# Kernel optimization log

Hardware: AMD Instinct MI355X
Metric: run time of the kernel (lower is better)

Reference implementation:

```python
import jax, jax.numpy as jnp
import numpy as np

HEADS = 8
DIM_HEAD = 64
KNN = 32
SCALE = DIM_HEAD ** -0.5


def setup_inputs() -> dict:
    key = jax.random.key(0)
    k1, k2, k3 = jax.random.split(key, 3)
    B, N, C = 2, 2048, 256
    inner = HEADS * DIM_HEAD  # 512
    x = jax.random.normal(k1, (B, N, C), dtype=jnp.float32)
    Wqkv = jax.random.normal(k2, (C, 3 * inner), dtype=jnp.float32) * (C ** -0.5)
    Wout = jax.random.normal(k3, (inner, C), dtype=jnp.float32) * (inner ** -0.5)
    bout = jnp.zeros((C,), dtype=jnp.float32)
    return {"x": x, "Wqkv": Wqkv, "Wout": Wout, "bout": bout}


def _knn_adjacency(x, k):
    # x: [B, N, C] -> boolean adjacency [B, N, N], k nearest neighbors by
    # euclidean distance, self-loops excluded (loop=False).
    B, N, _ = x.shape
    x2 = jnp.sum(x * x, axis=-1)  # [B, N]
    # squared distances [B, N, N]
    d2 = x2[:, :, None] + x2[:, None, :] - 2.0 * jnp.einsum('bnc,bmc->bnm', x, x)
    big = jnp.finfo(d2.dtype).max
    d2 = d2 + big * jnp.eye(N, dtype=d2.dtype)  # exclude self
    _, idx = jax.lax.top_k(-d2, k)  # [B, N, k] nearest neighbor indices

    rows = jnp.arange(N)[:, None]  # [N, 1]

    def scatter_one(idx_b):
        return jnp.zeros((N, N), dtype=bool).at[rows, idx_b].set(True)

    return jax.vmap(scatter_one)(idx)  # [B, N, N]


def reference(x, Wqkv, Wout, bout):
    B, N, C = x.shape
    adj = _knn_adjacency(x, KNN)  # [B, N, N] bool, shared across heads

    qkv = x @ Wqkv  # [B, N, 3*inner]
    q, k, v = jnp.split(qkv, 3, axis=-1)
    split_heads = lambda t: t.reshape(B, N, HEADS, DIM_HEAD).transpose(0, 2, 1, 3)
    q, k, v = split_heads(q), split_heads(k), split_heads(v)  # [B, H, N, d]

    dots = jnp.einsum('bhnd,bhmd->bhnm', q, k) * SCALE  # [B, H, N, N]
    dots = jnp.where(adj[:, None, :, :], dots, -jnp.inf)
    attn = jax.nn.softmax(dots, axis=-1)
    out = jnp.einsum('bhnm,bhmd->bhnd', attn, v)  # [B, H, N, d]
    out = out.transpose(0, 2, 1, 3).reshape(B, N, HEADS * DIM_HEAD)
    return out @ Wout + bout
```

## Files before the change

kernel.cpp:

```cpp
#include <hip/hip_runtime.h>
#include <hip/hip_bf16.h>
#include <hip/hip_fp16.h>

#define BATCH 2
#define NPTS  2048
#define CDIM  256
#define NHEAD 8
#define DHEAD 64
#define INNER 512
#define TRIPLE 1536
#define KNN   32
#define SCALE 0.125f

#define GRAM_ITEMS 272
#define QKV_ITEMS  384
#define TOTAL_ITEMS (GRAM_ITEMS + QKV_ITEMS)

typedef __attribute__((ext_vector_type(8))) short short8;
typedef __attribute__((ext_vector_type(4))) float floatx4;
typedef __attribute__((ext_vector_type(4))) unsigned short ushort4v;
typedef unsigned short ushort;

#define TW  32
#define TSZ (128*TW)

__device__ __forceinline__ unsigned bfsplit(float x) {
    unsigned u = __float_as_uint(x);
    unsigned r = u + 0x7fffu + ((u >> 16) & 1u);
    unsigned hs = r >> 16;
    float hf = __uint_as_float(hs << 16);
    float lo = x - hf;
    unsigned u2 = __float_as_uint(lo);
    unsigned r2 = u2 + 0x7fffu + ((u2 >> 16) & 1u);
    return (hs & 0xffffu) | (r2 & 0xffff0000u);
}

__device__ __forceinline__ void bfsplit3(float x, ushort* hh, ushort* ll, ushort* qq) {
    unsigned u = __float_as_uint(x);
    unsigned r = u + 0x7fffu + ((u >> 16) & 1u);
    unsigned hs = r >> 16;
    float hf = __uint_as_float(hs << 16);
    float d1 = x - hf;
    unsigned u2 = __float_as_uint(d1);
    unsigned r2 = u2 + 0x7fffu + ((u2 >> 16) & 1u);
    unsigned ls = r2 >> 16;
    float lf = __uint_as_float(ls << 16);
    float d2 = d1 - lf;
    unsigned u3 = __float_as_uint(d2);
    unsigned r3 = u3 + 0x7fffu + ((u3 >> 16) & 1u);
    *hh = (ushort)hs;
    *ll = (ushort)ls;
    *qq = (ushort)(r3 >> 16);
}

__device__ __forceinline__ ushort f2h(float f) {
    __half h = __float2half(f);
    return *reinterpret_cast<ushort*>(&h);
}
__device__ __forceinline__ float h2f(ushort u) {
    __half h;
    *reinterpret_cast<ushort*>(&h) = u;
    return __half2float(h);
}

__global__ __launch_bounds__(256) void input_prep_kernel(const float* __restrict__ x,
                                                         float* __restrict__ x2,
                                                         ushort* __restrict__ xhi,
                                                         ushort* __restrict__ xlo,
                                                         ushort* __restrict__ xqd) {
    int wave = threadIdx.x >> 6, lane = threadIdx.x & 63;
    int row = blockIdx.x * 4 + wave;
    const float* xr = x + (size_t)row * CDIM;
    float4 v = *(const float4*)(xr + lane * 4);
    float s = v.x*v.x + v.y*v.y + v.z*v.z + v.w*v.w;
    #pragma unroll
    for (int o = 32; o; o >>= 1) s += __shfl_down(s, o);
    if (lane == 0) x2[row] = s;

    ushort h[4], l[4], q[4];
    bfsplit3(v.x, &h[0], &l[0], &q[0]);
    bfsplit3(v.y, &h[1], &l[1], &q[1]);
    bfsplit3(v.z, &h[2], &l[2], &q[2]);
    bfsplit3(v.w, &h[3], &l[3], &q[3]);
    size_t off = (size_t)row * CDIM + lane * 4;
    *(ushort4v*)(xhi + off) = *(ushort4v*)h;
    *(ushort4v*)(xlo + off) = *(ushort4v*)l;
    *(ushort4v*)(xqd + off) = *(ushort4v*)q;
}

__global__ __launch_bounds__(256) void wtrans2_kernel(const float* __restrict__ Wqkv,
                                                      const float* __restrict__ Wout,
                                                      ushort* __restrict__ wqhiT,
                                                      ushort* __restrict__ wqloT,
                                                      ushort* __restrict__ wohiT,
                                                      ushort* __restrict__ woloT) {
    __shared__ float tile[64][65];
    const float* W; ushort* hiT; ushort* loT; int K, N, bx, by;
    int bid = blockIdx.x;
    if (bid < 96) { W = Wqkv; hiT = wqhiT; loT = wqloT; K = CDIM;  N = TRIPLE; bx = bid % 24; by = bid / 24; }
    else { int t = bid - 96; W = Wout; hiT = wohiT; loT = woloT; K = INNER; N = CDIM;  bx = t % 4;  by = t / 4; }
    int k0 = by * 64, n0 = bx * 64;
    #pragma unroll
    for (int i = 0; i < 4; ++i) {
        int f = threadIdx.x + i * 256;
        int r = f >> 4, c4 = (f & 15) * 4;
        float4 v = *(const float4*)(W + (size_t)(k0 + r) * N + n0 + c4);
        tile[r][c4+0] = v.x; tile[r][c4+1] = v.y;
        tile[r][c4+2] = v.z; tile[r][c4+3] = v.w;
    }
    __syncthreads();
    #pragma unroll
    for (int i = 0; i < 4; ++i) {
        int f = threadIdx.x + i * 256;
        int rn = f >> 4, ck = (f & 15) * 4;
        unsigned p0 = bfsplit(tile[ck+0][rn]);
        unsigned p1 = bfsplit(tile[ck+1][rn]);
        unsigned p2 = bfsplit(tile[ck+2][rn]);
        unsigned p3 = bfsplit(tile[ck+3][rn]);
        ushort4v h, l;
        h.x = (ushort)p0; l.x = (ushort)(p0 >> 16);
        h.y = (ushort)p1; l.y = (ushort)(p1 >> 16);
        h.z = (ushort)p2; l.z = (ushort)(p2 >> 16);
        h.w = (ushort)p3; l.w = (ushort)(p3 >> 16);
        *(ushort4v*)(hiT + (size_t)(n0 + rn) * K + k0 + ck) = h;
        *(ushort4v*)(loT + (size_t)(n0 + rn) * K + k0 + ck) = l;
    }
}


__device__ __forceinline__ void gemm_split_body(const ushort* __restrict__ Ahi,
                                                const ushort* __restrict__ Alo,
                                                const ushort* __restrict__ BhiT,
                                                const ushort* __restrict__ BloT,
                                                const float* __restrict__ bias,
                                                float* __restrict__ C,
                                                int N, int K, int bi, int bj,
                                                ushort* lds,
                                                ushort* __restrict__ kv16) {
    int lane = threadIdx.x & 63, wave = threadIdx.x >> 6;
    int wr = wave >> 1, wc = wave & 1;
    int fr = lane & 15, kg = lane >> 4;
    int swz8 = (kg ^ ((fr >> 1) & 3)) * 8;

    int srow = threadIdx.x >> 1;
    int hc = (threadIdx.x & 1) * 2;
    int sw = (srow >> 1) & 3;
    int d0 = srow * TW + ((hc + 0) ^ sw) * 8;
    int d1 = srow * TW + ((hc + 1) ^ sw) * 8;

    const ushort* g0 = Ahi  + (size_t)(bi + srow) * K + hc * 8;
    const ushort* g1 = Alo  + (size_t)(bi + srow) * K + hc * 8;
    const ushort* g2 = BhiT + (size_t)(bj + srow) * K + hc * 8;
    const ushort* g3 = BloT + (size_t)(bj + srow) * K + hc * 8;

    floatx4 acc[4][4] = {};

    for (int k0 = 0; k0 < K; k0 += 32) {
        uint4 va0 = *(const uint4*)(g0 + k0);
        uint4 va1 = *(const uint4*)(g0 + k0 + 8);
        uint4 vb0 = *(const uint4*)(g1 + k0);
        uint4 vb1 = *(const uint4*)(g1 + k0 + 8);
        uint4 vc0 = *(const uint4*)(g2 + k0);
        uint4 vc1 = *(const uint4*)(g2 + k0 + 8);
        uint4 vd0 = *(const uint4*)(g3 + k0);
        uint4 vd1 = *(const uint4*)(g3 + k0 + 8);
        *(uint4*)&lds[0*TSZ + d0] = va0;  *(uint4*)&lds[0*TSZ + d1] = va1;
        *(uint4*)&lds[1*TSZ + d0] = vb0;  *(uint4*)&lds[1*TSZ + d1] = vb1;
        *(uint4*)&lds[2*TSZ + d0] = vc0;  *(uint4*)&lds[2*TSZ + d1] = vc1;
        *(uint4*)&lds[3*TSZ + d0] = vd0;  *(uint4*)&lds[3*TSZ + d1] = vd1;
        __syncthreads();

        short8 a_h[4], a_l[4], b_h[4], b_l[4];
        #pragma unroll
        for (int m = 0; m < 4; ++m) {
            int off = (wr*64 + m*16 + fr) * TW + swz8;
            a_h[m] = *(const short8*)&lds[0*TSZ + off];
            a_l[m] = *(const short8*)&lds[1*TSZ + off];
        }
        #pragma unroll
        for (int n = 0; n < 4; ++n) {
            int off = (wc*64 + n*16 + fr) * TW + swz8;
            b_h[n] = *(const short8*)&lds[2*TSZ + off];
            b_l[n] = *(const short8*)&lds[3*TSZ + off];
        }
        #pragma unroll
        for (int m = 0; m < 4; ++m)
            #pragma unroll
            for (int n = 0; n < 4; ++n) {
                acc[m][n] = __builtin_amdgcn_mfma_f32_16x16x32_bf16(a_h[m], b_h[n], acc[m][n], 0, 0, 0);
                acc[m][n] = __builtin_amdgcn_mfma_f32_16x16x32_bf16(a_h[m], b_l[n], acc[m][n], 0, 0, 0);
                acc[m][n] = __builtin_amdgcn_mfma_f32_16x16x32_bf16(a_l[m], b_h[n], acc[m][n], 0, 0, 0);
            }
        __syncthreads();
    }

    if (kv16) {
        bool is_q = (bj < INNER);
        #pragma unroll
        for (int m = 0; m < 4; ++m)
            #pragma unroll
            for (int n = 0; n < 4; ++n) {
                int col = bj + wc*64 + n*16 + fr;
                #pragma unroll
                for (int r = 0; r < 4; ++r) {
                    int row = bi + wr*64 + m*16 + kg*4 + r;
                    float val = acc[m][n][r];
                    if (is_q) C[(size_t)row * INNER + col] = val;
                    else      kv16[(size_t)row * 1024 + (col - INNER)] = f2h(val);
                }
            }
    } else {
        #pragma unroll
        for (int m = 0; m < 4; ++m)
            #pragma unroll
            for (int n = 0; n < 4; ++n) {
                int col = bj + wc*64 + n*16 + fr;
                float bv = bias ? bias[col] : 0.0f;
                #pragma unroll
                for (int r = 0; r < 4; ++r) {
                    int row = bi + wr*64 + m*16 + kg*4 + r;
                    C[(size_t)row * N + col] = acc[m][n][r] + bv;
                }
            }
    }
}

__device__ __forceinline__ void gram_body(const ushort* __restrict__ Ah,
                                          const ushort* __restrict__ Al,
                                          const ushort* __restrict__ Aq,
                                          const float* __restrict__ x2b,
                                          float* __restrict__ Sb,
                                          int bi, int bj, ushort* lds) {
    int lane = threadIdx.x & 63, wave = threadIdx.x >> 6;
    int wr = wave >> 1, wc = wave & 1;
    int fr = lane & 15, kg = lane >> 4;
    int swz8 = (kg ^ ((fr >> 1) & 3)) * 8;

    int srow = threadIdx.x >> 1;
    int hc = (threadIdx.x & 1) * 2;
    int sw = (srow >> 1) & 3;
    int d0 = srow * TW + ((hc + 0) ^ sw) * 8;
    int d1 = srow * TW + ((hc + 1) ^ sw) * 8;

    const ushort* g0 = Ah + (size_t)(bi + srow) * CDIM + hc * 8;
    const ushort* g1 = Al + (size_t)(bi + srow) * CDIM + hc * 8;
    const ushort* g2 = Aq + (size_t)(bi + srow) * CDIM + hc * 8;
    const ushort* g3 = Ah + (size_t)(bj + srow) * CDIM + hc * 8;
    const ushort* g4 = Al + (size_t)(bj + srow) * CDIM + hc * 8;
    const ushort* g5 = Aq + (size_t)(bj + srow) * CDIM + hc * 8;

    floatx4 acc[4][4] = {};

    for (int k0 = 0; k0 < CDIM; k0 += 32) {
        uint4 a0 = *(const uint4*)(g0 + k0); uint4 a1 = *(const uint4*)(g0 + k0 + 8);
        uint4 b0 = *(const uint4*)(g1 + k0); uint4 b1 = *(const uint4*)(g1 + k0 + 8);
        uint4 c0 = *(const uint4*)(g2 + k0); uint4 c1 = *(const uint4*)(g2 + k0 + 8);
        uint4 e0 = *(const uint4*)(g3 + k0); uint4 e1 = *(const uint4*)(g3 + k0 + 8);
        uint4 f0 = *(const uint4*)(g4 + k0); uint4 f1 = *(const uint4*)(g4 + k0 + 8);
        uint4 h0 = *(const uint4*)(g5 + k0); uint4 h1 = *(const uint4*)(g5 + k0 + 8);
        *(uint4*)&lds[0*TSZ + d0] = a0; *(uint4*)&lds[0*TSZ + d1] = a1;
        *(uint4*)&lds[1*TSZ + d0] = b0; *(uint4*)&lds[1*TSZ + d1] = b1;
        *(uint4*)&lds[2*TSZ + d0] = c0; *(uint4*)&lds[2*TSZ + d1] = c1;
        *(uint4*)&lds[3*TSZ + d0] = e0; *(uint4*)&lds[3*TSZ + d1] = e1;
        *(uint4*)&lds[4*TSZ + d0] = f0; *(uint4*)&lds[4*TSZ + d1] = f1;
        *(uint4*)&lds[5*TSZ + d0] = h0; *(uint4*)&lds[5*TSZ + d1] = h1;
        __syncthreads();

        short8 a_h[4], a_l[4], a_q[4], b_h[4], b_l[4], b_q[4];
        #pragma unroll
        for (int m = 0; m < 4; ++m) {
            int off = (wr*64 + m*16 + fr) * TW + swz8;
            a_h[m] = *(const short8*)&lds[0*TSZ + off];
            a_l[m] = *(const short8*)&lds[1*TSZ + off];
            a_q[m] = *(const short8*)&lds[2*TSZ + off];
        }
        #pragma unroll
        for (int n = 0; n < 4; ++n) {
            int off = (wc*64 + n*16 + fr) * TW + swz8;
            b_h[n] = *(const short8*)&lds[3*TSZ + off];
            b_l[n] = *(const short8*)&lds[4*TSZ + off];
            b_q[n] = *(const short8*)&lds[5*TSZ + off];
        }
        #pragma unroll
        for (int m = 0; m < 4; ++m)
            #pragma unroll
            for (int n = 0; n < 4; ++n) {
                acc[m][n] = __builtin_amdgcn_mfma_f32_16x16x32_bf16(a_h[m], b_h[n], acc[m][n], 0, 0, 0);
                acc[m][n] = __builtin_amdgcn_mfma_f32_16x16x32_bf16(a_h[m], b_l[n], acc[m][n], 0, 0, 0);
                acc[m][n] = __builtin_amdgcn_mfma_f32_16x16x32_bf16(a_l[m], b_h[n], acc[m][n], 0, 0, 0);
                acc[m][n] = __builtin_amdgcn_mfma_f32_16x16x32_bf16(a_l[m], b_l[n], acc[m][n], 0, 0, 0);
                acc[m][n] = __builtin_amdgcn_mfma_f32_16x16x32_bf16(a_h[m], b_q[n], acc[m][n], 0, 0, 0);
                acc[m][n] = __builtin_amdgcn_mfma_f32_16x16x32_bf16(a_q[m], b_h[n], acc[m][n], 0, 0, 0);
            }
        __syncthreads();
    }

    #pragma unroll
    for (int m = 0; m < 4; ++m)
        #pragma unroll
        for (int n = 0; n < 4; ++n) {
            int col = bj + wc*64 + n*16 + fr;
            float xc = x2b[col];
            #pragma unroll
            for (int r = 0; r < 4; ++r) {
                int row = bi + wr*64 + m*16 + kg*4 + r;
                float val = xc - 2.0f * acc[m][n][r];
                if (row == col) val = __builtin_inff();
                Sb[(size_t)row * NPTS + col] = val;
            }
        }

    if (bi != bj) {
        float* T = (float*)lds;
        #pragma unroll
        for (int p = 0; p < 2; ++p) {
            __syncthreads();
            if (wc == p) {
                #pragma unroll
                for (int m = 0; m < 4; ++m) {
                    int row0 = wr*64 + m*16 + kg*4;
                    float x0 = x2b[bi + row0 + 0];
                    float x1 = x2b[bi + row0 + 1];
                    float x2v = x2b[bi + row0 + 2];
                    float x3 = x2b[bi + row0 + 3];
                    #pragma unroll
                    for (int n = 0; n < 4; ++n) {
                        int colp = n*16 + fr;
                        float4 v;
                        v.x = x0 - 2.0f * acc[m][n][0];
                        v.y = x1 - 2.0f * acc[m][n][1];
                        v.z = x2v - 2.0f * acc[m][n][2];
                        v.w = x3 - 2.0f * acc[m][n][3];
                        *(float4*)&T[colp * 132 + row0] = v;
                    }
                }
            }
            __syncthreads();
            #pragma unroll
            for (int i = 0; i < 8; ++i) {
                int f = threadIdx.x + i * 256;
                int cr = f >> 5, c4 = (f & 31) * 4;
                float4 v = *(const float4*)&T[cr * 132 + c4];
                *(float4*)(Sb + (size_t)(bj + p*64 + cr) * NPTS + bi + c4) = v;
            }
        }
    }
}

__global__ __launch_bounds__(256) void fused_mfma_kernel(const ushort* __restrict__ xh,
                                                         const ushort* __restrict__ xl,
                                                         const ushort* __restrict__ xq,
                                                         const float* __restrict__ x2,
                                                         float* __restrict__ S,
                                                         const ushort* __restrict__ wqhiT,
                                                         const ushort* __restrict__ wqloT,
                                                         float* __restrict__ q,
                                                         ushort* __restrict__ kv16) {
    __shared__ ushort lds[6*TSZ];
    int item = blockIdx.x;
    if (item < GRAM_ITEMS) {
        int b = item / 136, t = item % 136;
        int by = 0;
        while (t >= 16 - by) { t -= 16 - by; ++by; }
        int bx = by + t;
        size_t xoff = (size_t)b * NPTS * CDIM;
        gram_body(xh + xoff, xl + xoff, xq + xoff,
                  x2 + (size_t)b * NPTS, S + (size_t)b * NPTS * NPTS,
                  by * 128, bx * 128, lds);
    } else {
        int t = item - GRAM_ITEMS;
        int bx = t % 12, by = t / 12;
        gemm_split_body(xh, xl, wqhiT, wqloT, nullptr, q,
                        TRIPLE, CDIM, by * 128, bx * 128, lds, kv16);
    }
}

__global__ __launch_bounds__(256) void outproj_kernel(const ushort* __restrict__ Ahi,
                                                      const ushort* __restrict__ Alo,
                                                      const ushort* __restrict__ BhiT,
                                                      const ushort* __restrict__ BloT,
                                                      const float* __restrict__ bias,
                                                      float* __restrict__ C) {
    __shared__ ushort lds[4*TSZ];
    gemm_split_body(Ahi, Alo, BhiT, BloT, bias, C,
                    CDIM, INNER, blockIdx.y * 128, blockIdx.x * 128, lds, nullptr);
}

__device__ __forceinline__ unsigned block_excl_scan_256(unsigned c,
                                                        unsigned* wsum,
                                                        unsigned* total_out) {
    unsigned v = c;
    #pragma unroll
    for (int o = 1; o < 64; o <<= 1) {
        unsigned t = __shfl_up(v, o);
        if ((threadIdx.x & 63) >= o) v += t;
    }
    if ((threadIdx.x & 63) == 63) wsum[threadIdx.x >> 6] = v;
    __syncthreads();
    unsigned woff = 0;
    int mywave = threadIdx.x >> 6;
    #pragma unroll
    for (int w = 0; w < 4; ++w) {
        unsigned s = wsum[w];
        if (w < mywave) woff += s;
    }
    if (total_out) *total_out = wsum[0] + wsum[1] + wsum[2] + wsum[3];
    __syncthreads();
    return v + woff - c;
}

__global__ __launch_bounds__(256) void knn_attn_kernel(const float* __restrict__ S,
                                                       const float* __restrict__ q,
                                                       const ushort* __restrict__ kv16,
                                                       ushort* __restrict__ ahi,
                                                       ushort* __restrict__ alo) {
    int bid = blockIdx.x;
    int b = (bid & 7) >> 2;
    int n = ((bid >> 3) << 2) | (bid & 3);
    size_t rowoff = (size_t)b * NPTS + n;
    const float* row = S + rowoff * NPTS;

    __shared__ unsigned keys[NPTS];
    __shared__ unsigned hist[256];
    __shared__ unsigned wsum[4];
    __shared__ unsigned s_red[8];
    __shared__ unsigned sh_lo, sh_hi, sh_rank, sh_cnt, sh_break;
    __shared__ unsigned ckey[64];
    __shared__ int     cidx[64];
    __shared__ unsigned s_ccount;
    __shared__ int   nb[KNN];
    __shared__ float dots[NHEAD][KNN];
    __shared__ float p[NHEAD][KNN];

    int tid = threadIdx.x;

    unsigned mn = 0xffffffffu, mx = 0u;
    {
        int i0 = tid * 8;
        float4 f0 = *(const float4*)(row + i0);
        float4 f1 = *(const float4*)(row + i0 + 4);
        float fv[8] = { f0.x, f0.y, f0.z, f0.w, f1.x, f1.y, f1.z, f1.w };
        #pragma unroll
        for (int t = 0; t < 8; ++t) {
            int i = i0 + t;
            unsigned u;
            if (i == n) {
                u = 0xffffffffu;
            } else {
                unsigned v = __float_as_uint(fv[t]);
                u = (v & 0x80000000u) ? ~v : (v | 0x80000000u);
                mn = min(mn, u); mx = max(mx, u);
            }
            keys[i] = u;
        }
    }
    #pragma unroll
    for (int o = 32; o; o >>= 1) {
        mn = min(mn, (unsigned)__shfl_xor((int)mn, o));
        mx = max(mx, (unsigned)__shfl_xor((int)mx, o));
    }
    if ((tid & 63) == 0) { s_red[tid >> 6] = mn; s_red[4 + (tid >> 6)] = mx; }
    __syncthreads();
    if (tid == 0) {
        unsigned a = min(min(s_red[0], s_red[1]), min(s_red[2], s_red[3]));
        unsigned z = max(max(s_red[4], s_red[5]), max(s_red[6], s_red[7]));
        sh_lo = a; sh_hi = z; sh_rank = KNN; sh_break = 0; s_ccount = 0;
    }
    __syncthreads();

    for (int it = 0; it < 5; ++it) {
        unsigned lo = sh_lo, hi = sh_hi;
        unsigned range1 = hi - lo;
        int shift = 0;
        if (range1 > 255u) shift = 24 - __clz(range1);
        hist[tid] = 0;
        __syncthreads();
        for (int i = tid; i < NPTS; i += 256) {
            unsigned u = keys[i];
            if (u >= lo && u <= hi)
                atomicAdd(&hist[(u - lo) >> shift], 1u);
        }
        __syncthreads();
        unsigned c = hist[tid];
        unsigned rank = sh_rank;
        unsigned excl = block_excl_scan_256(c, wsum, nullptr);
        if (excl < rank && excl + c >= rank) {
            sh_rank = rank - excl;
            unsigned nlo = lo + ((unsigned)tid << shift);
            unsigned span = (shift == 0) ? 0u : (((1u << shift)) - 1u);
            unsigned nhi = nlo + span;
            if (nhi > hi || nhi < nlo) nhi = hi;
            sh_lo = nlo; sh_hi = nhi;
            sh_cnt = c;
            sh_break = (shift == 0 || c <= 64u) ? 1u : 0u;
        }
        __syncthreads();
        if (sh_break) break;
    }

    unsigned lo = sh_lo, hi = sh_hi, rank = sh_rank, cnt = sh_cnt;

    unsigned lt = 0;
    for (int i = tid; i < NPTS; i += 256) lt += (keys[i] < lo) ? 1u : 0u;
    unsigned pos = block_excl_scan_256(lt, wsum, nullptr);
    for (int i = tid; i < NPTS; i += 256) {
        unsigned u = keys[i];
        if (u < lo) nb[pos++] = i;
        else if (u >= lo && u <= hi && cnt <= 64u) {
            unsigned pp = atomicAdd(&s_ccount, 1u);
            ckey[pp] = u; cidx[pp] = i;
        }
    }
    __syncthreads();

    unsigned base = KNN - rank;
    if (cnt <= 64u) {
        if (tid < (int)cnt) {
            unsigned myk = ckey[tid]; int myi = cidx[tid];
            unsigned r = 0;
            for (unsigned s = 0; s < cnt; ++s) {
                unsigned sk = ckey[s]; int si = cidx[s];
                r += (sk < myk || (sk == myk && si < myi)) ? 1u : 0u;
            }
            if (r < rank) nb[base + r] = myi;
        }
    } else {
        if (tid == 0) {
            unsigned need = rank, pp = base;
            for (int i = 0; i < NPTS && need; ++i) {
                if (keys[i] >= lo && keys[i] <= hi) { nb[pp++] = i; --need; }
            }
        }
    }
    __syncthreads();

    const float* qrow = q + rowoff * INNER;
    const ushort* kvb = kv16 + (size_t)b * NPTS * 1024;

    {
        int j = tid >> 3;
        int l = tid & 7;
        const ushort* krow = kvb + (size_t)nb[j] * 1024 + l * 8;
        short8 kr[NHEAD];
        #pragma unroll
        for (int h = 0; h < NHEAD; ++h)
            kr[h] = *(const short8*)(krow + h * DHEAD);
        const float* qp = qrow + l * 8;
        #pragma unroll
        for (int h = 0; h < NHEAD; ++h) {
            float4 q0 = *(const float4*)(qp + h * DHEAD);
            float4 q1 = *(const float4*)(qp + h * DHEAD + 4);
            float d = h2f((ushort)kr[h][0]) * q0.x + h2f((ushort)kr[h][1]) * q0.y
                    + h2f((ushort)kr[h][2]) * q0.z + h2f((ushort)kr[h][3]) * q0.w
                    + h2f((ushort)kr[h][4]) * q1.x + h2f((ushort)kr[h][5]) * q1.y
                    + h2f((ushort)kr[h][6]) * q1.z + h2f((ushort)kr[h][7]) * q1.w;
            d += __shfl_xor(d, 1);
            d += __shfl_xor(d, 2);
            d += __shfl_xor(d, 4);
            if (l == 0) dots[h][j] = d * SCALE;
        }
    }
    __syncthreads();

    {
        int h = tid >> 5, jj = tid & 31;
        float dv = dots[h][jj];
        float mxv = dv;
        for (int o = 16; o; o >>= 1) mxv = fmaxf(mxv, __shfl_xor(mxv, o));
        float e = expf(dv - mxv);
        float s = e;
        for (int o = 16; o; o >>= 1) s += __shfl_xor(s, o);
        p[h][jj] = e / s;
    }
    __syncthreads();

    {
        int hd = tid >> 5;
        int jd = tid & 31;
        const ushort* vb = kvb + INNER + hd * DHEAD + jd * 2;
        float o0 = 0.f, o1 = 0.f;
        #pragma unroll
        for (int g = 0; g < 4; ++g) {
            unsigned vv[8]; float pw[8];
            #pragma unroll
            for (int t = 0; t < 8; ++t) {
                int jj = g * 8 + t;
                vv[t] = *(const unsigned*)(vb + (size_t)nb[jj] * 1024);
                pw[t] = p[hd][jj];
            }
            #pragma unroll
            for (int t = 0; t < 8; ++t) {
                o0 += pw[t] * h2f((ushort)(vv[t] & 0xffffu));
                o1 += pw[t] * h2f((ushort)(vv[t] >> 16));
            }
        }
        size_t baseo = rowoff * INNER + hd * DHEAD + jd * 2;
        unsigned q0 = bfsplit(o0);
        unsigned q1 = bfsplit(o1);
        *(unsigned*)(ahi + baseo) = (q0 & 0xffffu) | (q1 << 16);
        *(unsigned*)(alo + baseo) = (q0 >> 16) | (q1 & 0xffff0000u);
    }
}

extern "C" void kernel_launch(void* const* d_in, const int* in_sizes, int n_in,
                              void* d_out, int out_size, void* d_ws, size_t ws_size,
                              hipStream_t stream) {
    const float* x    = (const float*)d_in[0];
    const float* Wqkv = (const float*)d_in[1];
    const float* Wout = (const float*)d_in[2];
    const float* bout = (const float*)d_in[3];
    float* out = (float*)d_out;

    float* S     = (float*)d_ws;
    float* x2    = S + (size_t)BATCH * NPTS * NPTS;
    float* q     = x2 + (size_t)BATCH * NPTS;
    ushort* kv16 = (ushort*)(q + (size_t)BATCH * NPTS * INNER);
    ushort* xhi  = kv16 + (size_t)BATCH * NPTS * 1024;
    ushort* xlo   = xhi   + (size_t)BATCH * NPTS * CDIM;
    ushort* xqd   = xlo   + (size_t)BATCH * NPTS * CDIM;
    ushort* ahi   = xqd   + (size_t)BATCH * NPTS * CDIM;
    ushort* alo   = ahi   + (size_t)BATCH * NPTS * INNER;
    ushort* wqhiT = alo   + (size_t)BATCH * NPTS * INNER;
    ushort* wqloT = wqhiT + (size_t)TRIPLE * CDIM;
    ushort* wohiT = wqloT + (size_t)TRIPLE * CDIM;
    ushort* woloT = wohiT + (size_t)CDIM * INNER;

    input_prep_kernel<<<(BATCH * NPTS) / 4, 256, 0, stream>>>(x, x2, xhi, xlo, xqd);

    wtrans2_kernel<<<128, 256, 0, stream>>>(Wqkv, Wout, wqhiT, wqloT, wohiT, woloT);

    fused_mfma_kernel<<<TOTAL_ITEMS, 256, 0, stream>>>(xhi, xlo, xqd, x2, S,
                                                       wqhiT, wqloT, q, kv16);

    knn_attn_kernel<<<BATCH * NPTS, 256, 0, stream>>>(S, q, kv16, ahi, alo);

    {
        dim3 grid(CDIM / 128, (BATCH * NPTS) / 128);
        outproj_kernel<<<grid, 256, 0, stream>>>(ahi, alo, wohiT, woloT, bout, out);
    }
}
```

Baseline: 107.3 us.

## Load MFMA operands directly from global memory, drop LDS staging in GEMMs

The split-bf16 GEMM and Gram kernels no longer stage A/B tiles through shared memory with barriers. Each wave now loads its MFMA fragments straight from global memory (relying on L1/L2 for reuse across waves), and the k-loop is unrolled by two. LDS is kept only for the Gram mirror-transpose buffer. This removes LDS writes and the barriers inside the loop, but every operand is now read redundantly from global memory by the two waves that share it, using less coalesced 16-byte loads, which raises cache and memory traffic.

Measured after the change: 158.5 us. +47.7%, slower.

```diff
diff --git a/kernel.cpp b/kernel.cpp
--- a/kernel.cpp
+++ b/kernel.cpp
@@ -20,9 +20,6 @@
 typedef __attribute__((ext_vector_type(4))) float floatx4;
 typedef __attribute__((ext_vector_type(4))) unsigned short ushort4v;
 typedef unsigned short ushort;
-
-#define TW  32
-#define TSZ (128*TW)
 
 __device__ __forceinline__ unsigned bfsplit(float x) {
     unsigned u = __float_as_uint(x);
@@ -135,53 +132,32 @@
                                                 const float* __restrict__ bias,
                                                 float* __restrict__ C,
                                                 int N, int K, int bi, int bj,
-                                                ushort* lds,
                                                 ushort* __restrict__ kv16) {
     int lane = threadIdx.x & 63, wave = threadIdx.x >> 6;
     int wr = wave >> 1, wc = wave & 1;
     int fr = lane & 15, kg = lane >> 4;
-    int swz8 = (kg ^ ((fr >> 1) & 3)) * 8;
-
-    int srow = threadIdx.x >> 1;
-    int hc = (threadIdx.x & 1) * 2;
-    int sw = (srow >> 1) & 3;
-    int d0 = srow * TW + ((hc + 0) ^ sw) * 8;
-    int d1 = srow * TW + ((hc + 1) ^ sw) * 8;
-
-    const ushort* g0 = Ahi  + (size_t)(bi + srow) * K + hc * 8;
-    const ushort* g1 = Alo  + (size_t)(bi + srow) * K + hc * 8;
-    const ushort* g2 = BhiT + (size_t)(bj + srow) * K + hc * 8;
-    const ushort* g3 = BloT + (size_t)(bj + srow) * K + hc * 8;
+
+    const ushort* a0 = Ahi  + (size_t)(bi + wr*64 + fr) * K + kg*8;
+    const ushort* a1 = Alo  + (size_t)(bi + wr*64 + fr) * K + kg*8;
+    const ushort* b0 = BhiT + (size_t)(bj + wc*64 + fr) * K + kg*8;
+    const ushort* b1 = BloT + (size_t)(bj + wc*64 + fr) * K + kg*8;
 
     floatx4 acc[4][4] = {};
 
+    #pragma unroll 2
     for (int k0 = 0; k0 < K; k0 += 32) {
-        uint4 va0 = *(const uint4*)(g0 + k0);
-        uint4 va1 = *(const uint4*)(g0 + k0 + 8);
-        uint4 vb0 = *(const uint4*)(g1 + k0);
-        uint4 vb1 = *(const uint4*)(g1 + k0 + 8);
-        uint4 vc0 = *(const uint4*)(g2 + k0);
-        uint4 vc1 = *(const uint4*)(g2 + k0 + 8);
-        uint4 vd0 = *(const uint4*)(g3 + k0);
-        uint4 vd1 = *(const uint4*)(g3 + k0 + 8);
-        *(uint4*)&lds[0*TSZ + d0] = va0;  *(uint4*)&lds[0*TSZ + d1] = va1;
-        *(uint4*)&lds[1*TSZ + d0] = vb0;  *(uint4*)&lds[1*TSZ + d1] = vb1;
-        *(uint4*)&lds[2*TSZ + d0] = vc0;  *(uint4*)&lds[2*TSZ + d1] = vc1;
-        *(uint4*)&lds[3*TSZ + d0] = vd0;  *(uint4*)&lds[3*TSZ + d1] = vd1;
-        __syncthreads();
-
         short8 a_h[4], a_l[4], b_h[4], b_l[4];
         #pragma unroll
         for (int m = 0; m < 4; ++m) {
-            int off = (wr*64 + m*16 + fr) * TW + swz8;
-            a_h[m] = *(const short8*)&lds[0*TSZ + off];
-            a_l[m] = *(const short8*)&lds[1*TSZ + off];
+            size_t off = (size_t)(m*16) * K + k0;
+            a_h[m] = *(const short8*)(a0 + off);
+            a_l[m] = *(const short8*)(a1 + off);
         }
         #pragma unroll
         for (int n = 0; n < 4; ++n) {
-            int off = (wc*64 + n*16 + fr) * TW + swz8;
-            b_h[n] = *(const short8*)&lds[2*TSZ + off];
-            b_l[n] = *(const short8*)&lds[3*TSZ + off];
+            size_t off = (size_t)(n*16) * K + k0;
+            b_h[n] = *(const short8*)(b0 + off);
+            b_l[n] = *(const short8*)(b1 + off);
         }
         #pragma unroll
         for (int m = 0; m < 4; ++m)
@@ -191,7 +167,6 @@
                 acc[m][n] = __builtin_amdgcn_mfma_f32_16x16x32_bf16(a_h[m], b_l[n], acc[m][n], 0, 0, 0);
                 acc[m][n] = __builtin_amdgcn_mfma_f32_16x16x32_bf16(a_l[m], b_h[n], acc[m][n], 0, 0, 0);
             }
-        __syncthreads();
     }
 
     if (kv16) {
@@ -230,56 +205,36 @@
                                           const ushort* __restrict__ Aq,
                                           const float* __restrict__ x2b,
                                           float* __restrict__ Sb,
-                                          int bi, int bj, ushort* lds) {
+                                          int bi, int bj, float* Tmir) {
     int lane = threadIdx.x & 63, wave = threadIdx.x >> 6;
     int wr = wave >> 1, wc = wave & 1;
     int fr = lane & 15, kg = lane >> 4;
-    int swz8 = (kg ^ ((fr >> 1) & 3)) * 8;
-
-    int srow = threadIdx.x >> 1;
-    int hc = (threadIdx.x & 1) * 2;
-    int sw = (srow >> 1) & 3;
-    int d0 = srow * TW + ((hc + 0) ^ sw) * 8;
-    int d1 = srow * TW + ((hc + 1) ^ sw) * 8;
-
-    const ushort* g0 = Ah + (size_t)(bi + srow) * CDIM + hc * 8;
-    const ushort* g1 = Al + (size_t)(bi + srow) * CDIM + hc * 8;
-    const ushort* g2 = Aq + (size_t)(bi + srow) * CDIM + hc * 8;
-    const ushort* g3 = Ah + (size_t)(bj + srow) * CDIM + hc * 8;
-    const ushort* g4 = Al + (size_t)(bj + srow) * CDIM + hc * 8;
-    const ushort* g5 = Aq + (size_t)(bj + srow) * CDIM + hc * 8;
+
+    const ushort* a0 = Ah + (size_t)(bi + wr*64 + fr) * CDIM + kg*8;
+    const ushort* a1 = Al + (size_t)(bi + wr*64 + fr) * CDIM + kg*8;
+    const ushort* a2 = Aq + (size_t)(bi + wr*64 + fr) * CDIM + kg*8;
+    const ushort* b0 = Ah + (size_t)(bj + wc*64 + fr) * CDIM + kg*8;
+    const ushort* b1 = Al + (size_t)(bj + wc*64 + fr) * CDIM + kg*8;
+    const ushort* b2 = Aq + (size_t)(bj + wc*64 + fr) * CDIM + kg*8;
 
     floatx4 acc[4][4] = {};
 
+    #pragma unroll 2
     for (int k0 = 0; k0 < CDIM; k0 += 32) {
-        uint4 a0 = *(const uint4*)(g0 + k0); uint4 a1 = *(const uint4*)(g0 + k0 + 8);
-        uint4 b0 = *(const uint4*)(g1 + k0); uint4 b1 = *(const uint4*)(g1 + k0 + 8);
-        uint4 c0 = *(const uint4*)(g2 + k0); uint4 c1 = *(const uint4*)(g2 + k0 + 8);
-        uint4 e0 = *(const uint4*)(g3 + k0); uint4 e1 = *(const uint4*)(g3 + k0 + 8);
-        uint4 f0 = *(const uint4*)(g4 + k0); uint4 f1 = *(const uint4*)(g4 + k0 + 8);
-        uint4 h0 = *(const uint4*)(g5 + k0); uint4 h1 = *(const uint4*)(g5 + k0 + 8);
-        *(uint4*)&lds[0*TSZ + d0] = a0; *(uint4*)&lds[0*TSZ + d1] = a1;
-        *(uint4*)&lds[1*TSZ + d0] = b0; *(uint4*)&lds[1*TSZ + d1] = b1;
-        *(uint4*)&lds[2*TSZ + d0] = c0; *(uint4*)&lds[2*TSZ + d1] = c1;
-        *(uint4*)&lds[3*TSZ + d0] = e0; *(uint4*)&lds[3*TSZ + d1] = e1;
-        *(uint4*)&lds[4*TSZ + d0] = f0; *(uint4*)&lds[4*TSZ + d1] = f1;
-        *(uint4*)&lds[5*TSZ + d0] = h0; *(uint4*)&lds[5*TSZ + d1] = h1;
-        __syncthreads();
-
         short8 a_h[4], a_l[4], a_q[4], b_h[4], b_l[4], b_q[4];
         #pragma unroll
         for (int m = 0; m < 4; ++m) {
-            int off = (wr*64 + m*16 + fr) * TW + swz8;
-            a_h[m] = *(const short8*)&lds[0*TSZ + off];
-            a_l[m] = *(const short8*)&lds[1*TSZ + off];
-            a_q[m] = *(const short8*)&lds[2*TSZ + off];
+            size_t off = (size_t)(m*16) * CDIM + k0;
+            a_h[m] = *(const short8*)(a0 + off);
+            a_l[m] = *(const short8*)(a1 + off);
+            a_q[m] = *(const short8*)(a2 + off);
         }
         #pragma unroll
         for (int n = 0; n < 4; ++n) {
-            int off = (wc*64 + n*16 + fr) * TW + swz8;
-            b_h[n] = *(const short8*)&lds[3*TSZ + off];
-            b_l[n] = *(const short8*)&lds[4*TSZ + off];
-            b_q[n] = *(const short8*)&lds[5*TSZ + off];
+            size_t off = (size_t)(n*16) * CDIM + k0;
+            b_h[n] = *(const short8*)(b0 + off);
+            b_l[n] = *(const short8*)(b1 + off);
+            b_q[n] = *(const short8*)(b2 + off);
         }
         #pragma unroll
         for (int m = 0; m < 4; ++m)
@@ -292,7 +247,6 @@
                 acc[m][n] = __builtin_amdgcn_mfma_f32_16x16x32_bf16(a_h[m], b_q[n], acc[m][n], 0, 0, 0);
                 acc[m][n] = __builtin_amdgcn_mfma_f32_16x16x32_bf16(a_q[m], b_h[n], acc[m][n], 0, 0, 0);
             }
-        __syncthreads();
     }
 
     #pragma unroll
@@ -311,7 +265,7 @@
         }
 
     if (bi != bj) {
-        float* T = (float*)lds;
+        float* T = Tmir;
         #pragma unroll
         for (int p = 0; p < 2; ++p) {
             __syncthreads();
@@ -356,7 +310,7 @@
                                                          const ushort* __restrict__ wqloT,
                                                          float* __restrict__ q,
                                                          ushort* __restrict__ kv16) {
-    __shared__ ushort lds[6*TSZ];
+    __shared__ float Tmir[64*132];
     int item = blockIdx.x;
     if (item < GRAM_ITEMS) {
         int b = item / 136, t = item % 136;
@@ -366,12 +320,12 @@
         size_t xoff = (size_t)b * NPTS * CDIM;
         gram_body(xh + xoff, xl + xoff, xq + xoff,
                   x2 + (size_t)b * NPTS, S + (size_t)b * NPTS * NPTS,
-                  by * 128, bx * 128, lds);
+                  by * 128, bx * 128, Tmir);
     } else {
         int t = item - GRAM_ITEMS;
         int bx = t % 12, by = t / 12;
         gemm_split_body(xh, xl, wqhiT, wqloT, nullptr, q,
-                        TRIPLE, CDIM, by * 128, bx * 128, lds, kv16);
+                        TRIPLE, CDIM, by * 128, bx * 128, kv16);
     }
 }
 
@@ -381,9 +335,8 @@
                                                       const ushort* __restrict__ BloT,
                                                       const float* __restrict__ bias,
                                                       float* __restrict__ C) {
-    __shared__ ushort lds[4*TSZ];
     gemm_split_body(Ahi, Alo, BhiT, BloT, bias, C,
-                    CDIM, INNER, blockIdx.y * 128, blockIdx.x * 128, lds, nullptr);
+                    CDIM, INNER, blockIdx.y * 128, blockIdx.x * 128, nullptr);
 }
 
 __device__ __forceinline__ unsigned block_excl_scan_256(unsigned c,
```
